# Performance work log

Hardware: AMD Instinct MI355X
Metric: run time of the kernel (lower is better)

Reference implementation:

```python
import jax, jax.numpy as jnp
import numpy as np

# Model dims (match init_kwargs)
D_MODEL = 768
D_STATE = 128
HEADDIM = 64
EXPAND = 2
D_CONV = 4
D_INNER = EXPAND * D_MODEL              # 1536 (== d_ssm)
NHEADS = D_INNER // HEADDIM             # 24
CONV_DIM = D_INNER + 2 * D_STATE        # 1792
D_IN_PROJ = 2 * D_INNER + 2 * D_STATE + NHEADS  # 3352
BATCH, SEQLEN = 2, 512


def setup_inputs() -> dict:
    key = jax.random.key(0)
    ks = jax.random.split(key, 8)
    u = jax.random.normal(ks[0], (BATCH, SEQLEN, D_MODEL), jnp.float32)
    W_in = jax.random.normal(ks[1], (D_IN_PROJ, D_MODEL), jnp.float32) * 0.02
    conv_w = jax.random.normal(ks[2], (CONV_DIM, D_CONV), jnp.float32) * 0.3
    conv_b = jax.random.normal(ks[3], (CONV_DIM,), jnp.float32) * 0.1
    # dt_bias = inverse-softplus of dt sampled log-uniform in [dt_min, dt_max]
    dt = jnp.exp(jax.random.uniform(ks[4], (NHEADS,)) * (np.log(0.02) - np.log(1e-3)) + np.log(1e-3))
    dt_bias = dt + jnp.log(-jnp.expm1(-dt))
    A_log = jnp.log(jax.random.uniform(ks[5], (NHEADS,), minval=1.0, maxval=16.0))
    D_param = jnp.ones((NHEADS,), jnp.float32)
    W_out = jax.random.normal(ks[6], (D_MODEL, D_INNER), jnp.float32) * 0.02
    return dict(u=u, W_in=W_in, conv_w=conv_w, conv_b=conv_b,
                dt_bias=dt_bias, A_log=A_log, D_param=D_param, W_out=W_out)


def _mamba2_scan(u, W_in, conv_w, conv_b, dt_bias, A_log, D_param, W_out):
    B, L, _ = u.shape
    A = -jnp.exp(A_log)  # (H,)

    def step(carry, u_t):
        conv_state, ssm_state = carry  # (B, CONV_DIM, D_CONV), (B, H, P, N)
        zxbcdt = u_t @ W_in.T          # (B, D_IN_PROJ); d_mlp == 0
        z = zxbcdt[:, :D_INNER]
        xBC = zxbcdt[:, D_INNER:D_INNER + CONV_DIM]
        dt = zxbcdt[:, D_INNER + CONV_DIM:]
        # causal depthwise conv state update (roll + write last)
        conv_state = jnp.concatenate([conv_state[:, :, 1:], xBC[:, :, None]], axis=-1)
        xbc = jax.nn.silu(jnp.sum(conv_state * conv_w[None], axis=-1) + conv_b)
        x = xbc[:, :D_INNER]
        Bm = xbc[:, D_INNER:D_INNER + D_STATE]
        Cm = xbc[:, D_INNER + D_STATE:]
        dt = jax.nn.softplus(dt + dt_bias)          # (B, H)
        dA = jnp.exp(dt * A)                        # (B, H)
        xh = x.reshape(B, NHEADS, HEADDIM)          # (B, H, P)
        dBx = jnp.einsum('bh,bn,bhp->bhpn', dt, Bm, xh)
        ssm_state = ssm_state * dA[:, :, None, None] + dBx
        y = jnp.einsum('bhpn,bn->bhp', ssm_state, Cm) + D_param[None, :, None] * xh
        y = y.reshape(B, D_INNER) * jax.nn.silu(z)  # gate (rmsnorm=False)
        return (conv_state, ssm_state), y @ W_out.T

    init = (jnp.zeros((B, CONV_DIM, D_CONV), u.dtype),
            jnp.zeros((B, NHEADS, HEADDIM, D_STATE), u.dtype))
    _, ys = jax.lax.scan(jax.checkpoint(step), init, jnp.swapaxes(u, 0, 1))
    return jnp.swapaxes(ys, 0, 1)  # (B, L, D_MODEL)


def reference(u, W_in, conv_w, conv_b, dt_bias, A_log, D_param, W_out):
    return _mamba2_scan(u, W_in, conv_w, conv_b, dt_bias, A_log, D_param, W_out)
```

## Files before the change

### kernel.cpp

```cpp
#include <hip/hip_runtime.h>
#include <math.h>

#define B_     2
#define L_     512
#define DM     768
#define DS     128
#define HD     64
#define DI     1536
#define NH     24
#define CONVD  1792
#define DPROJ  3352
#define ML     (B_*L_)
#define Q      64
#define NC     (L_/Q)
#define NPAD1  3456

typedef __bf16 bf16x8 __attribute__((ext_vector_type(8)));
typedef float f32x4 __attribute__((ext_vector_type(4)));

__device__ __forceinline__ float sigmoidf_(float x){ return 1.f/(1.f+__expf(-x)); }
__device__ __forceinline__ ushort bf16rn(float x){
  uint u = __float_as_uint(x);
  u += 0x7fff + ((u>>16)&1);
  return (ushort)(u>>16);
}
__device__ __forceinline__ float bf2f(ushort h){ return __uint_as_float(((uint)h)<<16); }
__device__ __forceinline__ void gll16(const void* g, void* l){
  __builtin_amdgcn_global_load_lds((const __attribute__((address_space(1))) void*)g,
                                   (__attribute__((address_space(3))) void*)l, 16, 0, 0);
}

__launch_bounds__(256)
__global__ void cvt_split(const float* __restrict__ src, ushort* __restrict__ dst,
                          int Rsrc, int Rdst, int K){
  int idx = blockIdx.x*256 + threadIdx.x;
  int K4 = K>>2;
  if (idx >= Rdst*K4) return;
  int r = idx / K4, c = (idx - r*K4)<<2;
  float4 v = make_float4(0,0,0,0);
  if (r < Rsrc) v = *(const float4*)&src[(size_t)r*K + c];
  float xv[4] = {v.x,v.y,v.z,v.w};
  uint hp[2], lp[2];
  ushort h[4], l[4];
#pragma unroll
  for (int j=0;j<4;j++){ h[j]=bf16rn(xv[j]); l[j]=bf16rn(xv[j]-bf2f(h[j])); }
  hp[0] = (uint)h[0] | ((uint)h[1]<<16); hp[1] = (uint)h[2] | ((uint)h[3]<<16);
  lp[0] = (uint)l[0] | ((uint)l[1]<<16); lp[1] = (uint)l[2] | ((uint)l[3]<<16);
  *(uint2*)&dst[(size_t)r*2*K + c]     = make_uint2(hp[0],hp[1]);
  *(uint2*)&dst[(size_t)r*2*K + K + c] = make_uint2(lp[0],lp[1]);
}

template<int BM,int BN,int K,int SPLITK,bool ATOMIC>
__launch_bounds__(256, 2)
__global__ void gemm4(const ushort* __restrict__ AS, const ushort* __restrict__ BS,
                      float* __restrict__ C, int Nvalid, int Nstore){
  constexpr int KS = K / SPLITK;
  constexpr int STEPS = KS / 64;
  constexpr int WM=BM/2, WN=BN/2, FM=WM/16, FN=WN/16;
  __shared__ ushort Ah[2][BM*64], Alo[2][BM*64], Bh[2][BN*64], Blo[2][BN*64];
  const int tid=threadIdx.x, lane=tid&63, w=tid>>6;
  const int WR=w>>1, WC=w&1;
  const int bm=blockIdx.x*BM, bn=blockIdx.y*BN;
  const int kbase = blockIdx.z*KS;
  const int lr=lane&15;
  const int srow=lane>>3;
  const int scol=(((lane&7) ^ (srow&7))*8);
  f32x4 acc[FM][FN] = {};

  auto stage = [&](int d, int ks){
    int k0 = kbase + ks*64;
#pragma unroll
    for (int ci=w; ci<BM/8; ci+=4){
      size_t ro = (size_t)(bm + ci*8 + srow)*(2*K);
      gll16(&AS[ro + k0 + scol],     &Ah[d][ci*512]);
      gll16(&AS[ro + K + k0 + scol], &Alo[d][ci*512]);
    }
#pragma unroll
    for (int ci=w; ci<BN/8; ci+=4){
      size_t ro = (size_t)(bn + ci*8 + srow)*(2*K);
      gll16(&BS[ro + k0 + scol],     &Bh[d][ci*512]);
      gll16(&BS[ro + K + k0 + scol], &Blo[d][ci*512]);
    }
  };

  stage(0, 0);
  __syncthreads();
  int cur = 0;
  for (int ks=0; ks<STEPS; ks++){
    if (ks+1 < STEPS) stage(cur^1, ks+1);

    bf16x8 ah[2][FM], al[2][FM], bh[2][FN], bl[2][FN];
#pragma unroll
    for (int s2=0;s2<2;s2++){
      int gslot = s2*4 + (lane>>4);
#pragma unroll
      for (int i=0;i<FM;i++){
        int R = WR*WM + i*16 + lr;
        int so = (gslot ^ (lr&7))*8;
        ah[s2][i] = *(const bf16x8*)&Ah[cur][R*64 + so];
        al[s2][i] = *(const bf16x8*)&Alo[cur][R*64 + so];
      }
#pragma unroll
      for (int j=0;j<FN;j++){
        int R = WC*WN + j*16 + lr;
        int so = (gslot ^ (lr&7))*8;
        bh[s2][j] = *(const bf16x8*)&Bh[cur][R*64 + so];
        bl[s2][j] = *(const bf16x8*)&Blo[cur][R*64 + so];
      }
    }
#pragma unroll
    for (int s2=0;s2<2;s2++)
#pragma unroll
      for (int i=0;i<FM;i++)
#pragma unroll
        for (int j=0;j<FN;j++){
          acc[i][j] = __builtin_amdgcn_mfma_f32_16x16x32_bf16(ah[s2][i], bh[s2][j], acc[i][j], 0,0,0);
          acc[i][j] = __builtin_amdgcn_mfma_f32_16x16x32_bf16(ah[s2][i], bl[s2][j], acc[i][j], 0,0,0);
          acc[i][j] = __builtin_amdgcn_mfma_f32_16x16x32_bf16(al[s2][i], bh[s2][j], acc[i][j], 0,0,0);
        }

    __syncthreads();
    cur ^= 1;
  }

#pragma unroll
  for (int i=0;i<FM;i++)
#pragma unroll
    for (int j=0;j<FN;j++){
      int n = bn + WC*WN + j*16 + lr;
      if (n < Nvalid){
#pragma unroll
        for (int e=0;e<4;e++){
          int m = bm + WR*WM + i*16 + (lane>>4)*4 + e;
          if (ATOMIC) atomicAdd(&C[(size_t)m*Nstore + n], acc[i][j][e]);
          else        C[(size_t)m*Nstore + n] = acc[i][j][e];
        }
      }
    }
}

__launch_bounds__(256)
__global__ void conv2_kernel(const float* __restrict__ zx,
                             const float* __restrict__ cw,
                             const float* __restrict__ cb,
                             float* __restrict__ xbc){
  int g = blockIdx.x;
  int c = blockIdx.y;
  int b = blockIdx.z;
  int ch = g*256 + threadIdx.x;
  const float* src = zx + (size_t)(b*L_ + c*Q)*DPROJ + DI + ch;
  float* dst = xbc + (size_t)(b*L_ + c*Q)*CONVD + ch;
  float w0=cw[ch*4],w1=cw[ch*4+1],w2=cw[ch*4+2],w3=cw[ch*4+3],bias=cb[ch];
  float x0=0.f,x1=0.f,x2=0.f;
  if (c > 0){
    x0 = *(src - 3*DPROJ);
    x1 = *(src - 2*DPROJ);
    x2 = *(src - 1*DPROJ);
  }
#pragma unroll 4
  for (int tt=0; tt<Q; tt++){
    float xt = src[(size_t)tt*DPROJ];
    float a = bias;
    a = fmaf(w3, xt, a); a = fmaf(w2, x2, a); a = fmaf(w1, x1, a); a = fmaf(w0, x0, a);
    dst[(size_t)tt*CONVD] = a * sigmoidf_(a);
    x0 = x1; x1 = x2; x2 = xt;
  }
}

__launch_bounds__(64)
__global__ void dt_kernel(const float* __restrict__ zx,
                          const float* __restrict__ dt_bias,
                          const float* __restrict__ A_log,
                          float* __restrict__ dts, float* __restrict__ las){
  int blk = blockIdx.x;
  int c = blk % NC; int h = (blk/NC)%NH; int b = blk/(NC*NH);
  int lane = threadIdx.x;
  int t = c*Q + lane;
  float raw = zx[(size_t)(b*L_+t)*DPROJ + DI + CONVD + h] + dt_bias[h];
  float dtv = raw > 20.f ? raw : log1pf(__expf(raw));
  float A = -__expf(A_log[h]);
  float la = dtv * A;
#pragma unroll
  for (int off=1; off<64; off<<=1){
    float v = __shfl_up(la, off);
    if (lane >= off) la += v;
  }
  int idx = (b*NH+h)*L_ + t;
  dts[idx] = dtv;
  las[idx] = la;
}

__launch_bounds__(256)
__global__ void chunk_state_kernel(const float* __restrict__ xbc,
                                   const float* __restrict__ dts,
                                   const float* __restrict__ las,
                                   float* __restrict__ Schunk){
  __shared__ float Xw[Q][68];
  __shared__ float Bs[Q][132];
  int c = blockIdx.x, h = blockIdx.y, b = blockIdx.z;
  int tid = threadIdx.x;
  int bh = b*NH + h;
  const int tbase = bh*L_ + c*Q;
  float la63 = las[tbase + 63];

  for (int it = tid; it < Q*16; it += 256){
    int s = it >> 4, p4 = (it & 15) << 2;
    float4 v = *(const float4*)&xbc[(size_t)(b*L_ + c*Q + s)*CONVD + h*HD + p4];
    float w = __expf(la63 - las[tbase + s]) * dts[tbase + s];
    Xw[s][p4+0]=v.x*w; Xw[s][p4+1]=v.y*w; Xw[s][p4+2]=v.z*w; Xw[s][p4+3]=v.w*w;
  }
  for (int it = tid; it < Q*32; it += 256){
    int s = it >> 5, n4 = (it & 31) << 2;
    float4 v = *(const float4*)&xbc[(size_t)(b*L_ + c*Q + s)*CONVD + DI + n4];
    Bs[s][n4+0]=v.x; Bs[s][n4+1]=v.y; Bs[s][n4+2]=v.z; Bs[s][n4+3]=v.w;
  }
  __syncthreads();

  int ty = tid >> 4, tx = tid & 15;
  int p0 = ty*4;
  float acc[4][8] = {};
#pragma unroll 4
  for (int k=0;k<Q;k++){
    float4 a4 = *(const float4*)&Xw[k][p0];
    float4 b0 = *(const float4*)&Bs[k][tx*4];
    float4 b1 = *(const float4*)&Bs[k][64 + tx*4];
    float a[4]={a4.x,a4.y,a4.z,a4.w};
    float bb[8]={b0.x,b0.y,b0.z,b0.w,b1.x,b1.y,b1.z,b1.w};
#pragma unroll
    for(int i=0;i<4;i++)
#pragma unroll
      for(int j=0;j<8;j++) acc[i][j] = fmaf(a[i], bb[j], acc[i][j]);
  }
  float* Sb = Schunk + ((size_t)bh*NC + c)*(HD*DS);
#pragma unroll
  for(int i=0;i<4;i++){
    int p = p0+i;
    *(float4*)&Sb[p*DS + tx*4]      = make_float4(acc[i][0],acc[i][1],acc[i][2],acc[i][3]);
    *(float4*)&Sb[p*DS + 64 + tx*4] = make_float4(acc[i][4],acc[i][5],acc[i][6],acc[i][7]);
  }
}

__launch_bounds__(256)
__global__ void interchunk_kernel(float* __restrict__ S, const float* __restrict__ las){
  int blk = blockIdx.x;
  int slice = blk & 7; int bh = blk >> 3;
  size_t base = (size_t)bh*NC*(HD*DS) + slice*1024 + threadIdx.x*4;
  float4 run = make_float4(0,0,0,0);
#pragma unroll
  for (int c=0;c<NC;c++){
    float dec = __expf(las[bh*L_ + c*Q + 63]);
    float4 ch = *(float4*)(S + base + c*(HD*DS));
    *(float4*)(S + base + c*(HD*DS)) = run;
    run.x = fmaf(run.x, dec, ch.x);
    run.y = fmaf(run.y, dec, ch.y);
    run.z = fmaf(run.z, dec, ch.z);
    run.w = fmaf(run.w, dec, ch.w);
  }
}

__launch_bounds__(256)
__global__ void chunk_out_kernel(const float* __restrict__ zx,
                                 const float* __restrict__ xbc,
                                 const float* __restrict__ dts,
                                 const float* __restrict__ las,
                                 const float* __restrict__ Sstart,
                                 const float* __restrict__ Dp,
                                 ushort* __restrict__ yS){
  __shared__ float R1[8192];
  __shared__ float R2[8192];
  int c = blockIdx.x, hh = blockIdx.y, b = blockIdx.z;
  int tid = threadIdx.x;
  int bh = b*NH + hh;
  const int tbase = bh*L_ + c*Q;
  const float Dh = Dp[hh];
  int ty = tid >> 4, tx = tid & 15;
  int t0 = ty*4, p0 = tx*4;

  for (int it = tid; it < 64*32; it += 256){
    int t = it & 63, n4 = (it >> 6) << 2;
    float4 v = *(const float4*)&xbc[(size_t)(b*L_ + c*Q + t)*CONVD + DI + DS + n4];
    R1[(n4+0)*64 + t]=v.x; R1[(n4+1)*64 + t]=v.y; R1[(n4+2)*64 + t]=v.z; R1[(n4+3)*64 + t]=v.w;
  }
  const float* Sb = Sstart + ((size_t)bh*NC + c)*(HD*DS);
  for (int it = tid; it < 64*32; it += 256){
    int p = it & 63, n4 = (it >> 6) << 2;
    float4 v = *(const float4*)&Sb[p*DS + n4];
    R2[(n4+0)*64 + p]=v.x; R2[(n4+1)*64 + p]=v.y; R2[(n4+2)*64 + p]=v.z; R2[(n4+3)*64 + p]=v.w;
  }
  __syncthreads();

  float Yi[4][4] = {};
#pragma unroll 4
  for (int k=0;k<DS;k++){
    float4 a4 = *(const float4*)&R1[k*64 + t0];
    float4 b4 = *(const float4*)&R2[k*64 + p0];
    float a[4]={a4.x,a4.y,a4.z,a4.w}, bb[4]={b4.x,b4.y,b4.z,b4.w};
#pragma unroll
    for(int i=0;i<4;i++)
#pragma unroll
      for(int j=0;j<4;j++) Yi[i][j] = fmaf(a[i], bb[j], Yi[i][j]);
  }
  __syncthreads();

  for (int it = tid; it < 64*32; it += 256){
    int s = it & 63, n4 = (it >> 6) << 2;
    float4 v = *(const float4*)&xbc[(size_t)(b*L_ + c*Q + s)*CONVD + DI + n4];
    R2[(n4+0)*64 + s]=v.x; R2[(n4+1)*64 + s]=v.y; R2[(n4+2)*64 + s]=v.z; R2[(n4+3)*64 + s]=v.w;
  }
  __syncthreads();

  float E[4][4] = {};
#pragma unroll 4
  for (int k=0;k<DS;k++){
    float4 a4 = *(const float4*)&R1[k*64 + t0];
    float4 b4 = *(const float4*)&R2[k*64 + p0];
    float a[4]={a4.x,a4.y,a4.z,a4.w}, bb[4]={b4.x,b4.y,b4.z,b4.w};
#pragma unroll
    for(int i=0;i<4;i++)
#pragma unroll
      for(int j=0;j<4;j++) E[i][j] = fmaf(a[i], bb[j], E[i][j]);
  }
  __syncthreads();

  {
    float lat[4], lass[4], dtv[4];
#pragma unroll
    for(int i=0;i<4;i++) lat[i]  = las[tbase + t0 + i];
#pragma unroll
    for(int j=0;j<4;j++){ lass[j] = las[tbase + p0 + j]; dtv[j] = dts[tbase + p0 + j]; }
#pragma unroll
    for(int i=0;i<4;i++)
#pragma unroll
      for(int j=0;j<4;j++){
        int t = t0+i, s = p0+j;
        float g = 0.f;
        if (s <= t) g = __expf(lat[i] - lass[j]) * dtv[j] * E[i][j];
        R1[t*65 + s] = g;
      }
  }
  for (int it = tid; it < 64*16; it += 256){
    int s = it >> 4, p4 = (it & 15) << 2;
    float4 v = *(const float4*)&xbc[(size_t)(b*L_ + c*Q + s)*CONVD + hh*HD + p4];
    *(float4*)&R2[s*64 + p4] = v;
  }
  __syncthreads();

  float Yv[4][4] = {};
#pragma unroll 4
  for (int k=0;k<Q;k++){
    float g[4];
#pragma unroll
    for(int i=0;i<4;i++) g[i] = R1[(t0+i)*65 + k];
    float4 x4 = *(const float4*)&R2[k*64 + p0];
    float xx[4]={x4.x,x4.y,x4.z,x4.w};
#pragma unroll
    for(int i=0;i<4;i++)
#pragma unroll
      for(int j=0;j<4;j++) Yv[i][j] = fmaf(g[i], xx[j], Yv[i][j]);
  }

#pragma unroll
  for(int i=0;i<4;i++){
    int t = t0 + i;
    float cp = __expf(las[tbase + t]);
    size_t row = (size_t)(b*L_ + c*Q + t);
    float4 z4 = *(const float4*)&zx[row*DPROJ + hh*HD + p0];
    float zz[4]={z4.x,z4.y,z4.z,z4.w};
    ushort h4[4], l4[4];
#pragma unroll
    for(int j=0;j<4;j++){
      float xv = R2[t*64 + p0 + j];
      float y = fmaf(cp, Yi[i][j], Yv[i][j]) + Dh*xv;
      float o = y * (zz[j] * sigmoidf_(zz[j]));
      h4[j] = bf16rn(o);
      l4[j] = bf16rn(o - bf2f(h4[j]));
    }
    size_t o0 = row*(size_t)(2*DI) + hh*HD + p0;
    *(uint2*)&yS[o0]      = make_uint2((uint)h4[0]|((uint)h4[1]<<16), (uint)h4[2]|((uint)h4[3]<<16));
    *(uint2*)&yS[o0 + DI] = make_uint2((uint)l4[0]|((uint)l4[1]<<16), (uint)l4[2]|((uint)l4[3]<<16));
  }
}

extern "C" void kernel_launch(void* const* d_in, const int* in_sizes, int n_in,
                              void* d_out, int out_size, void* d_ws, size_t ws_size,
                              hipStream_t stream) {
  const float* u       = (const float*)d_in[0];
  const float* W_in    = (const float*)d_in[1];
  const float* conv_w  = (const float*)d_in[2];
  const float* conv_b  = (const float*)d_in[3];
  const float* dt_bias = (const float*)d_in[4];
  const float* A_log   = (const float*)d_in[5];
  const float* D_param = (const float*)d_in[6];
  const float* W_out   = (const float*)d_in[7];
  float* out = (float*)d_out;

  float* ws = (float*)d_ws;
  float* zx     = ws;
  float* xbc    = zx   + (size_t)ML*DPROJ;
  float* dts    = xbc  + (size_t)ML*CONVD;
  float* las    = dts  + (size_t)B_*NH*L_;
  float* Schunk = las  + (size_t)B_*NH*L_;
  ushort* uS    = (ushort*)(Schunk + (size_t)B_*NH*NC*HD*DS);
  ushort* yS    = uS;
  ushort* WinS  = yS + (size_t)ML*2*DI;
  ushort* WoutS = WinS;

  cvt_split<<<(ML*(DM/4)+255)/256, 256, 0, stream>>>(u, uS, ML, ML, DM);
  cvt_split<<<(NPAD1*(DM/4)+255)/256, 256, 0, stream>>>(W_in, WinS, DPROJ, NPAD1, DM);
  {
    dim3 grid(ML/64, NPAD1/64, 1);
    gemm4<64,64,DM,1,false><<<grid, 256, 0, stream>>>(uS, WinS, zx, DPROJ, DPROJ);
  }
  {
    dim3 grid(7, NC, B_);
    conv2_kernel<<<grid, 256, 0, stream>>>(zx, conv_w, conv_b, xbc);
  }
  dt_kernel<<<B_*NH*NC, 64, 0, stream>>>(zx, dt_bias, A_log, dts, las);
  {
    dim3 grid(NC, NH, B_);
    chunk_state_kernel<<<grid, 256, 0, stream>>>(xbc, dts, las, Schunk);
  }
  interchunk_kernel<<<B_*NH*8, 256, 0, stream>>>(Schunk, las);
  {
    dim3 grid(NC, NH, B_);
    chunk_out_kernel<<<grid, 256, 0, stream>>>(zx, xbc, dts, las, Schunk, D_param, yS);
  }
  cvt_split<<<(DM*(DI/4)+255)/256, 256, 0, stream>>>(W_out, WoutS, DM, DM, DI);
  hipMemsetAsync(d_out, 0, (size_t)out_size*sizeof(float), stream);
  {
    dim3 grid(ML/64, DM/64, 4);
    gemm4<64,64,DI,4,true><<<grid, 256, 0, stream>>>(yS, WoutS, out, DM, DM);
  }
}
```

Measured before the change: 200.1 us.

## Rewrite chunk output kernel with split-bf16 MFMA and halve conv chunk length

Replaces the scalar FP32 FMA chunk-output kernel with a 512-thread MFMA version. Each operand is split into high and low bf16 parts with three MFMAs per product to keep near-fp32 accuracy, and LDS tiles use XOR swizzling to avoid bank conflicts. The conv kernel now processes 32-timestep slices instead of 64, doubling its grid for more parallelism. Costs include extra conversion work, more LDS use and a dropped lo*lo term that slightly loosens precision.

```diff
diff --git a/kernel.cpp b/kernel.cpp
--- a/kernel.cpp
+++ b/kernel.cpp
@@ -145,20 +145,21 @@
                              const float* __restrict__ cb,
                              float* __restrict__ xbc){
   int g = blockIdx.x;
-  int c = blockIdx.y;
+  int c2 = blockIdx.y;
   int b = blockIdx.z;
+  int t0g = c2*32;
   int ch = g*256 + threadIdx.x;
-  const float* src = zx + (size_t)(b*L_ + c*Q)*DPROJ + DI + ch;
-  float* dst = xbc + (size_t)(b*L_ + c*Q)*CONVD + ch;
+  const float* src = zx + (size_t)(b*L_ + t0g)*DPROJ + DI + ch;
+  float* dst = xbc + (size_t)(b*L_ + t0g)*CONVD + ch;
   float w0=cw[ch*4],w1=cw[ch*4+1],w2=cw[ch*4+2],w3=cw[ch*4+3],bias=cb[ch];
   float x0=0.f,x1=0.f,x2=0.f;
-  if (c > 0){
+  if (t0g > 0){
     x0 = *(src - 3*DPROJ);
     x1 = *(src - 2*DPROJ);
     x2 = *(src - 1*DPROJ);
   }
 #pragma unroll 4
-  for (int tt=0; tt<Q; tt++){
+  for (int tt=0; tt<32; tt++){
     float xt = src[(size_t)tt*DPROJ];
     float a = bias;
     a = fmaf(w3, xt, a); a = fmaf(w2, x2, a); a = fmaf(w1, x1, a); a = fmaf(w0, x0, a);
@@ -258,126 +259,204 @@
   }
 }
 
-__launch_bounds__(256)
-__global__ void chunk_out_kernel(const float* __restrict__ zx,
-                                 const float* __restrict__ xbc,
-                                 const float* __restrict__ dts,
-                                 const float* __restrict__ las,
-                                 const float* __restrict__ Sstart,
-                                 const float* __restrict__ Dp,
-                                 ushort* __restrict__ yS){
-  __shared__ float R1[8192];
-  __shared__ float R2[8192];
+__launch_bounds__(512)
+__global__ void chunk_out_mfma(const float* __restrict__ zx,
+                               const float* __restrict__ xbc,
+                               const float* __restrict__ dts,
+                               const float* __restrict__ las,
+                               const float* __restrict__ Sstart,
+                               const float* __restrict__ Dp,
+                               ushort* __restrict__ yS){
+  constexpr int OC_HI = 0,      OC_LO = 8192;
+  constexpr int OP_HI = 16384,  OP_LO = 24576;
+  constexpr int OX_HI = 32768,  OX_LO = 36864;
+  constexpr int OG_HI = 40960,  OG_LO = 45056;
+  __shared__ ushort LDSU[49152];
+  __shared__ float La[64], Dt[64];
+
   int c = blockIdx.x, hh = blockIdx.y, b = blockIdx.z;
   int tid = threadIdx.x;
   int bh = b*NH + hh;
   const int tbase = bh*L_ + c*Q;
   const float Dh = Dp[hh];
-  int ty = tid >> 4, tx = tid & 15;
-  int t0 = ty*4, p0 = tx*4;
-
-  for (int it = tid; it < 64*32; it += 256){
-    int t = it & 63, n4 = (it >> 6) << 2;
+  const int lane = tid & 63, w = tid >> 6;
+  const int wr = w >> 2, wc = w & 3;
+  const int lr = lane & 15, lk = lane >> 4;
+
+  for (int it = tid; it < 64*32; it += 512){
+    int t = it >> 5, n4 = (it & 31) << 2;
     float4 v = *(const float4*)&xbc[(size_t)(b*L_ + c*Q + t)*CONVD + DI + DS + n4];
-    R1[(n4+0)*64 + t]=v.x; R1[(n4+1)*64 + t]=v.y; R1[(n4+2)*64 + t]=v.z; R1[(n4+3)*64 + t]=v.w;
+    float xv[4] = {v.x,v.y,v.z,v.w};
+    ushort h[4], l[4];
+#pragma unroll
+    for (int j=0;j<4;j++){ h[j]=bf16rn(xv[j]); l[j]=bf16rn(xv[j]-bf2f(h[j])); }
+    int idx = t*128 + (((n4>>3) ^ (t&7))<<3) + (n4&7);
+    *(uint2*)&LDSU[OC_HI + idx] = make_uint2((uint)h[0]|((uint)h[1]<<16), (uint)h[2]|((uint)h[3]<<16));
+    *(uint2*)&LDSU[OC_LO + idx] = make_uint2((uint)l[0]|((uint)l[1]<<16), (uint)l[2]|((uint)l[3]<<16));
   }
   const float* Sb = Sstart + ((size_t)bh*NC + c)*(HD*DS);
-  for (int it = tid; it < 64*32; it += 256){
-    int p = it & 63, n4 = (it >> 6) << 2;
+  for (int it = tid; it < 64*32; it += 512){
+    int p = it >> 5, n4 = (it & 31) << 2;
     float4 v = *(const float4*)&Sb[p*DS + n4];
-    R2[(n4+0)*64 + p]=v.x; R2[(n4+1)*64 + p]=v.y; R2[(n4+2)*64 + p]=v.z; R2[(n4+3)*64 + p]=v.w;
-  }
-  __syncthreads();
-
-  float Yi[4][4] = {};
-#pragma unroll 4
-  for (int k=0;k<DS;k++){
-    float4 a4 = *(const float4*)&R1[k*64 + t0];
-    float4 b4 = *(const float4*)&R2[k*64 + p0];
-    float a[4]={a4.x,a4.y,a4.z,a4.w}, bb[4]={b4.x,b4.y,b4.z,b4.w};
-#pragma unroll
-    for(int i=0;i<4;i++)
-#pragma unroll
-      for(int j=0;j<4;j++) Yi[i][j] = fmaf(a[i], bb[j], Yi[i][j]);
-  }
-  __syncthreads();
-
-  for (int it = tid; it < 64*32; it += 256){
-    int s = it & 63, n4 = (it >> 6) << 2;
-    float4 v = *(const float4*)&xbc[(size_t)(b*L_ + c*Q + s)*CONVD + DI + n4];
-    R2[(n4+0)*64 + s]=v.x; R2[(n4+1)*64 + s]=v.y; R2[(n4+2)*64 + s]=v.z; R2[(n4+3)*64 + s]=v.w;
-  }
-  __syncthreads();
-
-  float E[4][4] = {};
-#pragma unroll 4
-  for (int k=0;k<DS;k++){
-    float4 a4 = *(const float4*)&R1[k*64 + t0];
-    float4 b4 = *(const float4*)&R2[k*64 + p0];
-    float a[4]={a4.x,a4.y,a4.z,a4.w}, bb[4]={b4.x,b4.y,b4.z,b4.w};
-#pragma unroll
-    for(int i=0;i<4;i++)
-#pragma unroll
-      for(int j=0;j<4;j++) E[i][j] = fmaf(a[i], bb[j], E[i][j]);
-  }
-  __syncthreads();
-
-  {
-    float lat[4], lass[4], dtv[4];
-#pragma unroll
-    for(int i=0;i<4;i++) lat[i]  = las[tbase + t0 + i];
-#pragma unroll
-    for(int j=0;j<4;j++){ lass[j] = las[tbase + p0 + j]; dtv[j] = dts[tbase + p0 + j]; }
-#pragma unroll
-    for(int i=0;i<4;i++)
-#pragma unroll
-      for(int j=0;j<4;j++){
-        int t = t0+i, s = p0+j;
-        float g = 0.f;
-        if (s <= t) g = __expf(lat[i] - lass[j]) * dtv[j] * E[i][j];
-        R1[t*65 + s] = g;
-      }
-  }
-  for (int it = tid; it < 64*16; it += 256){
+    float xv[4] = {v.x,v.y,v.z,v.w};
+    ushort h[4], l[4];
+#pragma unroll
+    for (int j=0;j<4;j++){ h[j]=bf16rn(xv[j]); l[j]=bf16rn(xv[j]-bf2f(h[j])); }
+    int idx = p*128 + (((n4>>3) ^ (p&7))<<3) + (n4&7);
+    *(uint2*)&LDSU[OP_HI + idx] = make_uint2((uint)h[0]|((uint)h[1]<<16), (uint)h[2]|((uint)h[3]<<16));
+    *(uint2*)&LDSU[OP_LO + idx] = make_uint2((uint)l[0]|((uint)l[1]<<16), (uint)l[2]|((uint)l[3]<<16));
+  }
+  for (int it = tid; it < 64*16; it += 512){
     int s = it >> 4, p4 = (it & 15) << 2;
     float4 v = *(const float4*)&xbc[(size_t)(b*L_ + c*Q + s)*CONVD + hh*HD + p4];
-    *(float4*)&R2[s*64 + p4] = v;
-  }
-  __syncthreads();
-
-  float Yv[4][4] = {};
-#pragma unroll 4
-  for (int k=0;k<Q;k++){
-    float g[4];
-#pragma unroll
-    for(int i=0;i<4;i++) g[i] = R1[(t0+i)*65 + k];
-    float4 x4 = *(const float4*)&R2[k*64 + p0];
-    float xx[4]={x4.x,x4.y,x4.z,x4.w};
-#pragma unroll
-    for(int i=0;i<4;i++)
-#pragma unroll
-      for(int j=0;j<4;j++) Yv[i][j] = fmaf(g[i], xx[j], Yv[i][j]);
-  }
-
-#pragma unroll
-  for(int i=0;i<4;i++){
-    int t = t0 + i;
-    float cp = __expf(las[tbase + t]);
-    size_t row = (size_t)(b*L_ + c*Q + t);
-    float4 z4 = *(const float4*)&zx[row*DPROJ + hh*HD + p0];
-    float zz[4]={z4.x,z4.y,z4.z,z4.w};
-    ushort h4[4], l4[4];
-#pragma unroll
-    for(int j=0;j<4;j++){
-      float xv = R2[t*64 + p0 + j];
-      float y = fmaf(cp, Yi[i][j], Yv[i][j]) + Dh*xv;
-      float o = y * (zz[j] * sigmoidf_(zz[j]));
-      h4[j] = bf16rn(o);
-      l4[j] = bf16rn(o - bf2f(h4[j]));
-    }
-    size_t o0 = row*(size_t)(2*DI) + hh*HD + p0;
-    *(uint2*)&yS[o0]      = make_uint2((uint)h4[0]|((uint)h4[1]<<16), (uint)h4[2]|((uint)h4[3]<<16));
-    *(uint2*)&yS[o0 + DI] = make_uint2((uint)l4[0]|((uint)l4[1]<<16), (uint)l4[2]|((uint)l4[3]<<16));
+    float xv[4] = {v.x,v.y,v.z,v.w};
+#pragma unroll
+    for (int j=0;j<4;j++){
+      int p = p4 + j;
+      ushort h = bf16rn(xv[j]);
+      ushort l = bf16rn(xv[j] - bf2f(h));
+      int idx = p*64 + (((s>>3) ^ (p&7))<<3) + (s&7);
+      LDSU[OX_HI + idx] = h; LDSU[OX_LO + idx] = l;
+    }
+  }
+  if (tid < 64){ La[tid] = las[tbase + tid]; Dt[tid] = dts[tbase + tid]; }
+  __syncthreads();
+
+  f32x4 yi[2] = {}, ev[2] = {}, yv[2] = {};
+
+#pragma unroll
+  for (int ks=0; ks<4; ks++){
+    bf16x8 ah[2], al[2], bh, bl;
+#pragma unroll
+    for (int fi=0; fi<2; fi++){
+      int R = wr*32 + fi*16 + lr;
+      int idx = R*128 + (((ks*4 + lk) ^ (R&7))<<3);
+      ah[fi] = *(const bf16x8*)&LDSU[OC_HI + idx];
+      al[fi] = *(const bf16x8*)&LDSU[OC_LO + idx];
+    }
+    { int Rb = wc*16 + lr;
+      int idx = Rb*128 + (((ks*4 + lk) ^ (Rb&7))<<3);
+      bh = *(const bf16x8*)&LDSU[OP_HI + idx];
+      bl = *(const bf16x8*)&LDSU[OP_LO + idx]; }
+#pragma unroll
+    for (int fi=0; fi<2; fi++){
+      yi[fi] = __builtin_amdgcn_mfma_f32_16x16x32_bf16(ah[fi], bh, yi[fi], 0,0,0);
+      yi[fi] = __builtin_amdgcn_mfma_f32_16x16x32_bf16(ah[fi], bl, yi[fi], 0,0,0);
+      yi[fi] = __builtin_amdgcn_mfma_f32_16x16x32_bf16(al[fi], bh, yi[fi], 0,0,0);
+    }
+  }
+  __syncthreads();
+
+  for (int it = tid; it < 64*32; it += 512){
+    int s = it >> 5, n4 = (it & 31) << 2;
+    float4 v = *(const float4*)&xbc[(size_t)(b*L_ + c*Q + s)*CONVD + DI + n4];
+    float xv[4] = {v.x,v.y,v.z,v.w};
+    ushort h[4], l[4];
+#pragma unroll
+    for (int j=0;j<4;j++){ h[j]=bf16rn(xv[j]); l[j]=bf16rn(xv[j]-bf2f(h[j])); }
+    int idx = s*128 + (((n4>>3) ^ (s&7))<<3) + (n4&7);
+    *(uint2*)&LDSU[OP_HI + idx] = make_uint2((uint)h[0]|((uint)h[1]<<16), (uint)h[2]|((uint)h[3]<<16));
+    *(uint2*)&LDSU[OP_LO + idx] = make_uint2((uint)l[0]|((uint)l[1]<<16), (uint)l[2]|((uint)l[3]<<16));
+  }
+  __syncthreads();
+
+#pragma unroll
+  for (int ks=0; ks<4; ks++){
+    bf16x8 ah[2], al[2], bh, bl;
+#pragma unroll
+    for (int fi=0; fi<2; fi++){
+      int R = wr*32 + fi*16 + lr;
+      int idx = R*128 + (((ks*4 + lk) ^ (R&7))<<3);
+      ah[fi] = *(const bf16x8*)&LDSU[OC_HI + idx];
+      al[fi] = *(const bf16x8*)&LDSU[OC_LO + idx];
+    }
+    { int Rb = wc*16 + lr;
+      int idx = Rb*128 + (((ks*4 + lk) ^ (Rb&7))<<3);
+      bh = *(const bf16x8*)&LDSU[OP_HI + idx];
+      bl = *(const bf16x8*)&LDSU[OP_LO + idx]; }
+#pragma unroll
+    for (int fi=0; fi<2; fi++){
+      ev[fi] = __builtin_amdgcn_mfma_f32_16x16x32_bf16(ah[fi], bh, ev[fi], 0,0,0);
+      ev[fi] = __builtin_amdgcn_mfma_f32_16x16x32_bf16(ah[fi], bl, ev[fi], 0,0,0);
+      ev[fi] = __builtin_amdgcn_mfma_f32_16x16x32_bf16(al[fi], bh, ev[fi], 0,0,0);
+    }
+  }
+
+  {
+    int s_col = wc*16 + lr;
+    float las_s = La[s_col], dt_s = Dt[s_col];
+#pragma unroll
+    for (int fi=0; fi<2; fi++)
+#pragma unroll
+      for (int e=0; e<4; e++){
+        int t = wr*32 + fi*16 + lk*4 + e;
+        float g = 0.f;
+        if (s_col <= t) g = __expf(La[t] - las_s) * dt_s * ev[fi][e];
+        ushort hg = bf16rn(g);
+        ushort lg = bf16rn(g - bf2f(hg));
+        int idx = t*64 + (((s_col>>3) ^ (t&7))<<3) + (s_col&7);
+        LDSU[OG_HI + idx] = hg; LDSU[OG_LO + idx] = lg;
+      }
+  }
+  __syncthreads();
+
+#pragma unroll
+  for (int ks=0; ks<2; ks++){
+    bf16x8 ah[2], al[2], bh, bl;
+#pragma unroll
+    for (int fi=0; fi<2; fi++){
+      int R = wr*32 + fi*16 + lr;
+      int idx = R*64 + (((ks*4 + lk) ^ (R&7))<<3);
+      ah[fi] = *(const bf16x8*)&LDSU[OG_HI + idx];
+      al[fi] = *(const bf16x8*)&LDSU[OG_LO + idx];
+    }
+    { int Rb = wc*16 + lr;
+      int idx = Rb*64 + (((ks*4 + lk) ^ (Rb&7))<<3);
+      bh = *(const bf16x8*)&LDSU[OX_HI + idx];
+      bl = *(const bf16x8*)&LDSU[OX_LO + idx]; }
+#pragma unroll
+    for (int fi=0; fi<2; fi++){
+      yv[fi] = __builtin_amdgcn_mfma_f32_16x16x32_bf16(ah[fi], bh, yv[fi], 0,0,0);
+      yv[fi] = __builtin_amdgcn_mfma_f32_16x16x32_bf16(ah[fi], bl, yv[fi], 0,0,0);
+      yv[fi] = __builtin_amdgcn_mfma_f32_16x16x32_bf16(al[fi], bh, yv[fi], 0,0,0);
+    }
+  }
+  __syncthreads();
+
+  {
+    float* Yf = (float*)&LDSU[OG_HI];
+    int p = wc*16 + lr;
+#pragma unroll
+    for (int fi=0; fi<2; fi++)
+#pragma unroll
+      for (int e=0; e<4; e++){
+        int t = wr*32 + fi*16 + lk*4 + e;
+        Yf[t*64 + p] = __expf(La[t])*yi[fi][e] + yv[fi][e];
+      }
+  }
+  __syncthreads();
+
+  {
+    const float* Yf = (const float*)&LDSU[OG_HI];
+    for (int it = tid; it < 64*16; it += 512){
+      int t = it >> 4, p4 = (it & 15) << 2;
+      size_t row = (size_t)(b*L_ + c*Q + t);
+      float4 x4 = *(const float4*)&xbc[row*CONVD + hh*HD + p4];
+      float4 z4 = *(const float4*)&zx[row*DPROJ + hh*HD + p4];
+      float xx[4] = {x4.x,x4.y,x4.z,x4.w};
+      float zz[4] = {z4.x,z4.y,z4.z,z4.w};
+      ushort h4[4], l4[4];
+#pragma unroll
+      for (int j=0;j<4;j++){
+        float y = Yf[t*64 + p4 + j] + Dh*xx[j];
+        float o = y * (zz[j] * sigmoidf_(zz[j]));
+        h4[j] = bf16rn(o);
+        l4[j] = bf16rn(o - bf2f(h4[j]));
+      }
+      size_t o0 = row*(size_t)(2*DI) + hh*HD + p4;
+      *(uint2*)&yS[o0]      = make_uint2((uint)h4[0]|((uint)h4[1]<<16), (uint)h4[2]|((uint)h4[3]<<16));
+      *(uint2*)&yS[o0 + DI] = make_uint2((uint)l4[0]|((uint)l4[1]<<16), (uint)l4[2]|((uint)l4[3]<<16));
+    }
   }
 }
 
@@ -412,7 +491,7 @@
     gemm4<64,64,DM,1,false><<<grid, 256, 0, stream>>>(uS, WinS, zx, DPROJ, DPROJ);
   }
   {
-    dim3 grid(7, NC, B_);
+    dim3 grid(7, L_/32, B_);
     conv2_kernel<<<grid, 256, 0, stream>>>(zx, conv_w, conv_b, xbc);
   }
   dt_kernel<<<B_*NH*NC, 64, 0, stream>>>(zx, dt_bias, A_log, dts, las);
@@ -423,7 +502,7 @@
   interchunk_kernel<<<B_*NH*8, 256, 0, stream>>>(Schunk, las);
   {
     dim3 grid(NC, NH, B_);
-    chunk_out_kernel<<<grid, 256, 0, stream>>>(zx, xbc, dts, las, Schunk, D_param, yS);
+    chunk_out_mfma<<<grid, 512, 0, stream>>>(zx, xbc, dts, las, Schunk, D_param, yS);
   }
   cvt_split<<<(DM*(DI/4)+255)/256, 256, 0, stream>>>(W_out, WoutS, DM, DM, DI);
   hipMemsetAsync(d_out, 0, (size_t)out_size*sizeof(float), stream);
```

New measurement: 183.4 us. 8.3% less time.
